# Optimization experiments

Hardware: AMD Instinct MI355X
Metric: run time of the kernel (lower is better)

Reference implementation:

```python
import math
import jax, jax.numpy as jnp
import numpy as np

B, T, H, DH, DV = 4, 4096, 16, 128, 128
CHUNK = 1024
ROPE_BASE = 10000.0
NEG = -1e30


def setup_inputs() -> dict:
    key = jax.random.key(0)
    kq, kk, kv = jax.random.split(key, 3)
    q = jax.random.normal(kq, (B, T, H, DH), dtype=jnp.float32)
    k = jax.random.normal(kk, (B, T, H, DH), dtype=jnp.float32)
    v = jax.random.normal(kv, (B, T, H, DV), dtype=jnp.float32)
    return {"q": q, "k": k, "v": v, "start_index": 0}


def _rope_tables(start, length, dh):
    half = dh // 2
    inv_freq = jnp.exp(jnp.arange(half, dtype=jnp.float32) * -(math.log(ROPE_BASE) / half))
    pos = start + jnp.arange(length, dtype=jnp.float32)
    ang = pos[:, None] * inv_freq[None, :]  # (T, half)
    # broadcast over batch and heads: (1, T, 1, half)
    return jnp.cos(ang)[None, :, None, :], jnp.sin(ang)[None, :, None, :]


def _rotate(x, cos, sin):
    x1, x2 = jnp.split(x, 2, axis=-1)
    return jnp.concatenate([x1 * cos - x2 * sin, x2 * cos + x1 * sin], axis=-1)


def reference(q, k, v, start_index):
    b, t, h, dh = q.shape
    dv = v.shape[-1]
    cos, sin = _rope_tables(start_index, t, dh)
    q_rot = _rotate(q, cos, sin)
    k_rot = _rotate(k, cos, sin)

    nc = t // CHUNK
    qc = q_rot.reshape(b, nc, CHUNK, h, dh)
    kc = k_rot.reshape(b, nc, CHUNK, h, dh)
    vc = v.reshape(b, nc, CHUNK, h, dv)

    # Normalized attention: no 1/sqrt(d) temperature (scale = 1.0)
    scores = jnp.einsum("bnqhd,bnkhd->bnhqk", qc, kc)
    causal = jnp.tril(jnp.ones((CHUNK, CHUNK), dtype=bool))
    scores = jnp.where(causal, scores, NEG)
    attn = jax.nn.softmax(scores, axis=-1)
    out = jnp.einsum("bnhqk,bnkhd->bnqhd", attn, vc)
    return out.reshape(b, t, h, dv)
```

## Files before the change

### kernel.cpp

```cpp
#include <hip/hip_runtime.h>
#include <math.h>

#define Tsz 4096
#define Hn 16
#define DHc 128
#define DVc 128
#define CHK 1024
#define NEGV (-1e30f)
#define ROPE_C 0.14391156831f

typedef float f32x4 __attribute__((ext_vector_type(4)));
typedef short s16x8 __attribute__((ext_vector_type(8)));
typedef unsigned short u16t;
typedef u16t u16x8 __attribute__((ext_vector_type(8)));

__device__ __forceinline__ u16t f2bf(float x){
  union { float f; unsigned u; } cv; cv.f = x;
  unsigned r = cv.u + 0x7fffu + ((cv.u >> 16) & 1u);
  return (u16t)(r >> 16);
}
__device__ __forceinline__ float bf2f(u16t h){
  union { float f; unsigned u; } cv; cv.u = ((unsigned)h) << 16;
  return cv.f;
}
__device__ __forceinline__ f32x4 mfma16(u16x8 a, u16x8 b, f32x4 c){
  return __builtin_amdgcn_mfma_f32_16x16x32_bf16(
      __builtin_bit_cast(s16x8, a), __builtin_bit_cast(s16x8, b), c, 0, 0, 0);
}

__global__ void rope_table_kernel(const int* __restrict__ start,
                                  float* __restrict__ tab){
  const int idx = blockIdx.x * 256 + threadIdx.x;
  const int t = idx >> 6, d = idx & 63;
  const float inv = expf(-(float)d * ROPE_C);
  const float ang = (float)(start[0] + t) * inv;
  float s, c;
  sincosf(ang, &s, &c);
  tab[idx] = c;
  tab[Tsz * 64 + idx] = s;
}

template<int MODE>
__global__ __launch_bounds__(512, 2)
void mega_attn_kernel(const float* __restrict__ q, const float* __restrict__ k,
                      const float* __restrict__ v, const float* __restrict__ tab,
                      const int* __restrict__ start, float* __restrict__ out)
{
  __shared__ __align__(16) u16t sKhi[64 * 128];
  __shared__ __align__(16) u16t sKlo[64 * 128];
  __shared__ __align__(16) u16t sVhi[128 * 64];
  __shared__ __align__(16) u16t sVlo[128 * 64];
  __shared__ __align__(16) u16t sP[8][2048];

  const int bid  = blockIdx.x;
  const int xcd  = bid & 7;
  const int jj   = bid >> 3;
  const int prob = xcd * 32 + (jj & 31);
  const int qt   = jj >> 5;
  const int b  = prob >> 6;
  const int ch = (prob >> 4) & 3;
  const int h  = prob & 15;

  const int tid  = threadIdx.x;
  const int w    = tid >> 6;
  const int lane = tid & 63;
  const int g    = lane >> 4;
  const int lc   = lane & 15;

  const float* cosT = tab;
  const float* sinT = tab + (size_t)Tsz * 64;
  const int tab0 = ch * CHK;
  int st = 0;
  if constexpr (MODE == 1) st = start[0];

  const size_t bh = ((size_t)b * Tsz + (size_t)ch * CHK) * Hn + h;
  const float* qbase = q + bh * DHc;
  const float* kbase = k + bh * DHc;
  const float* vbase = v + bh * DVc;
  float* obase = out + bh * DVc;
  const int rs = Hn * DHc;

  const int qrow0 = 256 * qt + 32 * w;
  u16t* myP = &sP[w][0];

  u16x8 qhi[2][4], qlo[2][4];
  {
    const int srow = lane >> 2;
    const int c4   = lane & 3;
    const int swz  = (srow & 7) << 3;
    #pragma unroll
    for (int rt = 0; rt < 2; ++rt){
      const int rck = qrow0 + rt * 16 + srow;
      const float* qp = qbase + (size_t)rck * rs + 16 * c4;
      f32x4 A[4], Bv[4], Cv[4], Sv[4];
      #pragma unroll
      for (int m = 0; m < 4; ++m){
        A[m]  = *(const f32x4*)(qp + 4 * m);
        Bv[m] = *(const f32x4*)(qp + 64 + 4 * m);
      }
      if constexpr (MODE == 0){
        const float* cp = cosT + (size_t)(tab0 + rck) * 64 + 16 * c4;
        const float* sp = sinT + (size_t)(tab0 + rck) * 64 + 16 * c4;
        #pragma unroll
        for (int m = 0; m < 4; ++m){
          Cv[m] = *(const f32x4*)(cp + 4 * m);
          Sv[m] = *(const f32x4*)(sp + 4 * m);
        }
      } else {
        const float pbase = (float)(st + tab0 + rck);
        #pragma unroll
        for (int m = 0; m < 16; ++m){
          const float inv = expf(-(float)(16 * c4 + m) * ROPE_C);
          float ss, cc;
          sincosf(pbase * inv, &ss, &cc);
          Cv[m >> 2][m & 3] = cc;
          Sv[m >> 2][m & 3] = ss;
        }
      }
      float r1[16], r2[16];
      u16t h1[16], h2[16];
      #pragma unroll
      for (int m = 0; m < 16; ++m){
        const float xa = A[m >> 2][m & 3];
        const float xb = Bv[m >> 2][m & 3];
        const float co = Cv[m >> 2][m & 3];
        const float si = Sv[m >> 2][m & 3];
        r1[m] = xa * co - xb * si;
        r2[m] = xb * co + xa * si;
        h1[m] = f2bf(r1[m]);
        h2[m] = f2bf(r2[m]);
      }
      u16x8 w0, w1, w2, w3;
      #pragma unroll
      for (int m = 0; m < 8; ++m){
        w0[m] = h1[m]; w1[m] = h1[m + 8];
        w2[m] = h2[m]; w3[m] = h2[m + 8];
      }
      *(u16x8*)(myP + ((srow * 128 + 16 * c4     ) ^ swz)) = w0;
      *(u16x8*)(myP + ((srow * 128 + 16 * c4 + 8 ) ^ swz)) = w1;
      *(u16x8*)(myP + ((srow * 128 + 16 * c4 + 64) ^ swz)) = w2;
      *(u16x8*)(myP + ((srow * 128 + 16 * c4 + 72) ^ swz)) = w3;
      #pragma unroll
      for (int ks = 0; ks < 4; ++ks)
        qhi[rt][ks] = *(const u16x8*)(myP + ((lc * 128 + ks * 32 + g * 8) ^ ((lc & 7) << 3)));
      #pragma unroll
      for (int m = 0; m < 8; ++m){
        w0[m] = f2bf(r1[m]     - bf2f(h1[m]));
        w1[m] = f2bf(r1[m + 8] - bf2f(h1[m + 8]));
        w2[m] = f2bf(r2[m]     - bf2f(h2[m]));
        w3[m] = f2bf(r2[m + 8] - bf2f(h2[m + 8]));
      }
      *(u16x8*)(myP + ((srow * 128 + 16 * c4     ) ^ swz)) = w0;
      *(u16x8*)(myP + ((srow * 128 + 16 * c4 + 8 ) ^ swz)) = w1;
      *(u16x8*)(myP + ((srow * 128 + 16 * c4 + 64) ^ swz)) = w2;
      *(u16x8*)(myP + ((srow * 128 + 16 * c4 + 72) ^ swz)) = w3;
      #pragma unroll
      for (int ks = 0; ks < 4; ++ks)
        qlo[rt][ks] = *(const u16x8*)(myP + ((lc * 128 + ks * 32 + g * 8) ^ ((lc & 7) << 3)));
    }
  }

  const f32x4 vzero = {0.f, 0.f, 0.f, 0.f};
  f32x4 acc[2][8];
  #pragma unroll
  for (int rt = 0; rt < 2; ++rt)
    #pragma unroll
    for (int dt = 0; dt < 8; ++dt) acc[rt][dt] = vzero;
  float mrow[8], lrow[8];
  #pragma unroll
  for (int i = 0; i < 8; ++i){ mrow[i] = -INFINITY; lrow[i] = 0.f; }

  const int ntiles = 4 * (qt + 1);
  const int krow = tid >> 3;
  const int kj   = tid & 7;

  for (int t = 0; t < ntiles; ++t){
    {
      const int kr = t * 64 + krow;
      const float* kp = kbase + (size_t)kr * rs + 8 * kj;
      f32x4 xa0 = *(const f32x4*)(kp);
      f32x4 xa1 = *(const f32x4*)(kp + 4);
      f32x4 xb0 = *(const f32x4*)(kp + 64);
      f32x4 xb1 = *(const f32x4*)(kp + 68);
      f32x4 c0, c1, s0, s1;
      if constexpr (MODE == 0){
        const float* cp = cosT + (size_t)(tab0 + kr) * 64 + 8 * kj;
        const float* sp = sinT + (size_t)(tab0 + kr) * 64 + 8 * kj;
        c0 = *(const f32x4*)(cp); c1 = *(const f32x4*)(cp + 4);
        s0 = *(const f32x4*)(sp); s1 = *(const f32x4*)(sp + 4);
      } else {
        const float pbase = (float)(st + tab0 + kr);
        #pragma unroll
        for (int m = 0; m < 8; ++m){
          const float inv = expf(-(float)(8 * kj + m) * ROPE_C);
          float ss, cc;
          sincosf(pbase * inv, &ss, &cc);
          if (m < 4){ c0[m] = cc; s0[m] = ss; }
          else      { c1[m - 4] = cc; s1[m - 4] = ss; }
        }
      }
      u16x8 hh1, ll1, hh2, ll2;
      #pragma unroll
      for (int m = 0; m < 8; ++m){
        const float xa = (m < 4) ? xa0[m & 3] : xa1[m & 3];
        const float xb = (m < 4) ? xb0[m & 3] : xb1[m & 3];
        const float co = (m < 4) ? c0[m & 3]  : c1[m & 3];
        const float si = (m < 4) ? s0[m & 3]  : s1[m & 3];
        const float r1 = xa * co - xb * si;
        const float r2 = xb * co + xa * si;
        const u16t a1h = f2bf(r1); hh1[m] = a1h; ll1[m] = f2bf(r1 - bf2f(a1h));
        const u16t a2h = f2bf(r2); hh2[m] = a2h; ll2[m] = f2bf(r2 - bf2f(a2h));
      }
      const int sw = (krow & 7) << 3;
      const int e1 = (krow * 128 + 8 * kj) ^ sw;
      const int e2 = (krow * 128 + 8 * kj + 64) ^ sw;
      *(u16x8*)(sKhi + e1) = hh1; *(u16x8*)(sKlo + e1) = ll1;
      *(u16x8*)(sKhi + e2) = hh2; *(u16x8*)(sKlo + e2) = ll2;

      const float* vp = vbase + (size_t)(t * 64 + krow) * rs + 16 * kj;
      f32x4 v0 = *(const f32x4*)(vp);
      f32x4 v1 = *(const f32x4*)(vp + 4);
      f32x4 v2 = *(const f32x4*)(vp + 8);
      f32x4 v3 = *(const f32x4*)(vp + 12);
      #pragma unroll
      for (int m = 0; m < 16; ++m){
        const int dv = 16 * kj + m;
        const float xv = (m < 4) ? v0[m & 3] : (m < 8) ? v1[m & 3]
                        : (m < 12) ? v2[m & 3] : v3[m & 3];
        const u16t vh = f2bf(xv);
        const int ve = (dv * 64 + krow) ^ ((((dv & 7) ^ ((dv >> 3) & 7))) << 3);
        sVhi[ve] = vh;
        sVlo[ve] = f2bf(xv - bf2f(vh));
      }
    }
    __syncthreads();

    const int kmin = t * 64;
    if (kmin <= qrow0 + 31){
      f32x4 S[2][4];
      #pragma unroll
      for (int ct = 0; ct < 4; ++ct){
        f32x4 s0v = vzero, s1v = vzero;
        const int krw = 16 * ct + lc;
        const int swk = (krw & 7) << 3;
        #pragma unroll
        for (int ks = 0; ks < 4; ++ks){
          const int ke = (krw * 128 + 32 * ks + 8 * g) ^ swk;
          const u16x8 bh = *(const u16x8*)(sKhi + ke);
          const u16x8 bl = *(const u16x8*)(sKlo + ke);
          s0v = mfma16(qhi[0][ks], bh, s0v);
          s0v = mfma16(qlo[0][ks], bh, s0v);
          s0v = mfma16(qhi[0][ks], bl, s0v);
          s1v = mfma16(qhi[1][ks], bh, s1v);
          s1v = mfma16(qlo[1][ks], bh, s1v);
          s1v = mfma16(qhi[1][ks], bl, s1v);
        }
        S[0][ct] = s0v; S[1][ct] = s1v;
      }
      if (kmin + 63 > qrow0){
        #pragma unroll
        for (int rt = 0; rt < 2; ++rt)
          #pragma unroll
          for (int ct = 0; ct < 4; ++ct){
            const int key = kmin + 16 * ct + lc;
            #pragma unroll
            for (int i = 0; i < 4; ++i){
              if (key > qrow0 + 16 * rt + 4 * g + i) S[rt][ct][i] = NEGV;
            }
          }
      }
      #pragma unroll
      for (int rt = 0; rt < 2; ++rt){
        #pragma unroll
        for (int i = 0; i < 4; ++i){
          const int idx = rt * 4 + i;
          float tm = fmaxf(fmaxf(S[rt][0][i], S[rt][1][i]),
                           fmaxf(S[rt][2][i], S[rt][3][i]));
          tm = fmaxf(tm, __shfl_xor(tm, 1));
          tm = fmaxf(tm, __shfl_xor(tm, 2));
          tm = fmaxf(tm, __shfl_xor(tm, 4));
          tm = fmaxf(tm, __shfl_xor(tm, 8));
          const float mnew = fmaxf(mrow[idx], tm);
          const float sc = __expf(mrow[idx] - mnew);
          float ps = 0.f;
          u16t pb[4];
          #pragma unroll
          for (int ct = 0; ct < 4; ++ct){
            const float p = __expf(S[rt][ct][i] - mnew);
            ps += p;
            pb[ct] = f2bf(p);
          }
          ps += __shfl_xor(ps, 1);
          ps += __shfl_xor(ps, 2);
          ps += __shfl_xor(ps, 4);
          ps += __shfl_xor(ps, 8);
          lrow[idx] = lrow[idx] * sc + ps;
          mrow[idx] = mnew;
          #pragma unroll
          for (int dt = 0; dt < 8; ++dt) acc[rt][dt][i] *= sc;
          const int prow = 16 * rt + 4 * g + i;
          const int swp = (prow & 7) << 3;
          #pragma unroll
          for (int ct = 0; ct < 4; ++ct)
            myP[(prow * 64 + 16 * ct + lc) ^ swp] = pb[ct];
        }
      }
      #pragma unroll
      for (int kvs = 0; kvs < 2; ++kvs){
        const u16x8 pa0 = *(const u16x8*)(myP + ((lc * 64 + kvs * 32 + 8 * g) ^ ((lc & 7) << 3)));
        const u16x8 pa1 = *(const u16x8*)(myP + (((16 + lc) * 64 + kvs * 32 + 8 * g) ^ ((lc & 7) << 3)));
        #pragma unroll
        for (int dt = 0; dt < 8; ++dt){
          const int dv = 16 * dt + lc;
          const int ve = (dv * 64 + kvs * 32 + 8 * g) ^ (((dv & 7) ^ ((dv >> 3) & 7)) << 3);
          const u16x8 vh = *(const u16x8*)(sVhi + ve);
          const u16x8 vl = *(const u16x8*)(sVlo + ve);
          acc[0][dt] = mfma16(pa0, vh, acc[0][dt]);
          acc[0][dt] = mfma16(pa0, vl, acc[0][dt]);
          acc[1][dt] = mfma16(pa1, vh, acc[1][dt]);
          acc[1][dt] = mfma16(pa1, vl, acc[1][dt]);
        }
      }
    }
    __syncthreads();
  }

  #pragma unroll
  for (int rt = 0; rt < 2; ++rt){
    #pragma unroll
    for (int i = 0; i < 4; ++i){
      const int idx = rt * 4 + i;
      const float rl = 1.f / lrow[idx];
      const int rck = qrow0 + 16 * rt + 4 * g + i;
      float* op = obase + (size_t)rck * rs + lc;
      #pragma unroll
      for (int dt = 0; dt < 8; ++dt)
        op[16 * dt] = acc[rt][dt][i] * rl;
    }
  }
}

extern "C" void kernel_launch(void* const* d_in, const int* in_sizes, int n_in,
                              void* d_out, int out_size, void* d_ws, size_t ws_size,
                              hipStream_t stream) {
  const float* q = (const float*)d_in[0];
  const float* k = (const float*)d_in[1];
  const float* v = (const float*)d_in[2];
  const int* start = (const int*)d_in[3];
  float* out = (float*)d_out;
  float* tab = (float*)d_ws;

  const size_t need = (size_t)2 * Tsz * 64 * sizeof(float);
  if (ws_size >= need){
    rope_table_kernel<<<dim3((Tsz * 64) / 256), dim3(256), 0, stream>>>(start, tab);
    mega_attn_kernel<0><<<dim3(1024), dim3(512), 0, stream>>>(q, k, v, tab, start, out);
  } else {
    mega_attn_kernel<1><<<dim3(1024), dim3(512), 0, stream>>>(q, k, v, tab, start, out);
  }
}
```

Before: 1.449 ms.

## Use 16 waves per block with 16 query rows per wave

Doubles the block to 1024 threads so each of 16 waves owns 16 query rows instead of 32. This halves per-wave register state and spreads the K/V tile staging over more threads. Q staging now borrows the K/V shared buffers as scratch, with a barrier before the main loop, which shrinks the P buffer. The cost is that each K/V tile is shared by more waves that each do less MFMA work, plus more barrier participants. Launch bounds of (1024,4) may force register spilling.

```diff
diff --git a/kernel.cpp b/kernel.cpp
--- a/kernel.cpp
+++ b/kernel.cpp
@@ -13,6 +13,7 @@
 typedef short s16x8 __attribute__((ext_vector_type(8)));
 typedef unsigned short u16t;
 typedef u16t u16x8 __attribute__((ext_vector_type(8)));
+typedef u16t u16x4 __attribute__((ext_vector_type(4)));
 
 __device__ __forceinline__ u16t f2bf(float x){
   union { float f; unsigned u; } cv; cv.f = x;
@@ -41,7 +42,7 @@
 }
 
 template<int MODE>
-__global__ __launch_bounds__(512, 2)
+__global__ __launch_bounds__(1024, 4)
 void mega_attn_kernel(const float* __restrict__ q, const float* __restrict__ k,
                       const float* __restrict__ v, const float* __restrict__ tab,
                       const int* __restrict__ start, float* __restrict__ out)
@@ -50,7 +51,7 @@
   __shared__ __align__(16) u16t sKlo[64 * 128];
   __shared__ __align__(16) u16t sVhi[128 * 64];
   __shared__ __align__(16) u16t sVlo[128 * 64];
-  __shared__ __align__(16) u16t sP[8][2048];
+  __shared__ __align__(16) u16t sP[16][1024];
 
   const int bid  = blockIdx.x;
   const int xcd  = bid & 7;
@@ -80,153 +81,138 @@
   float* obase = out + bh * DVc;
   const int rs = Hn * DHc;
 
-  const int qrow0 = 256 * qt + 32 * w;
+  const int qrow0 = 256 * qt + 16 * w;
   u16t* myP = &sP[w][0];
 
-  u16x8 qhi[2][4], qlo[2][4];
+  u16t* qscratch = (w < 4 ? sKhi : w < 8 ? sKlo : w < 12 ? sVhi : sVlo)
+                   + (size_t)(w & 3) * 2048;
+
+  u16x8 qhi[4], qlo[4];
   {
     const int srow = lane >> 2;
     const int c4   = lane & 3;
     const int swz  = (srow & 7) << 3;
-    #pragma unroll
-    for (int rt = 0; rt < 2; ++rt){
-      const int rck = qrow0 + rt * 16 + srow;
-      const float* qp = qbase + (size_t)rck * rs + 16 * c4;
-      f32x4 A[4], Bv[4], Cv[4], Sv[4];
+    const int rck = qrow0 + srow;
+    const float* qp = qbase + (size_t)rck * rs + 16 * c4;
+    f32x4 A[4], Bv[4], Cv[4], Sv[4];
+    #pragma unroll
+    for (int m = 0; m < 4; ++m){
+      A[m]  = *(const f32x4*)(qp + 4 * m);
+      Bv[m] = *(const f32x4*)(qp + 64 + 4 * m);
+    }
+    if constexpr (MODE == 0){
+      const float* cp = cosT + (size_t)(tab0 + rck) * 64 + 16 * c4;
+      const float* sp = sinT + (size_t)(tab0 + rck) * 64 + 16 * c4;
       #pragma unroll
       for (int m = 0; m < 4; ++m){
-        A[m]  = *(const f32x4*)(qp + 4 * m);
-        Bv[m] = *(const f32x4*)(qp + 64 + 4 * m);
-      }
-      if constexpr (MODE == 0){
-        const float* cp = cosT + (size_t)(tab0 + rck) * 64 + 16 * c4;
-        const float* sp = sinT + (size_t)(tab0 + rck) * 64 + 16 * c4;
-        #pragma unroll
-        for (int m = 0; m < 4; ++m){
-          Cv[m] = *(const f32x4*)(cp + 4 * m);
-          Sv[m] = *(const f32x4*)(sp + 4 * m);
-        }
-      } else {
-        const float pbase = (float)(st + tab0 + rck);
-        #pragma unroll
-        for (int m = 0; m < 16; ++m){
-          const float inv = expf(-(float)(16 * c4 + m) * ROPE_C);
-          float ss, cc;
-          sincosf(pbase * inv, &ss, &cc);
-          Cv[m >> 2][m & 3] = cc;
-          Sv[m >> 2][m & 3] = ss;
-        }
-      }
-      float r1[16], r2[16];
-      u16t h1[16], h2[16];
+        Cv[m] = *(const f32x4*)(cp + 4 * m);
+        Sv[m] = *(const f32x4*)(sp + 4 * m);
+      }
+    } else {
+      const float pbase = (float)(st + tab0 + rck);
       #pragma unroll
       for (int m = 0; m < 16; ++m){
-        const float xa = A[m >> 2][m & 3];
-        const float xb = Bv[m >> 2][m & 3];
-        const float co = Cv[m >> 2][m & 3];
-        const float si = Sv[m >> 2][m & 3];
-        r1[m] = xa * co - xb * si;
-        r2[m] = xb * co + xa * si;
-        h1[m] = f2bf(r1[m]);
-        h2[m] = f2bf(r2[m]);
-      }
-      u16x8 w0, w1, w2, w3;
-      #pragma unroll
-      for (int m = 0; m < 8; ++m){
-        w0[m] = h1[m]; w1[m] = h1[m + 8];
-        w2[m] = h2[m]; w3[m] = h2[m + 8];
-      }
-      *(u16x8*)(myP + ((srow * 128 + 16 * c4     ) ^ swz)) = w0;
-      *(u16x8*)(myP + ((srow * 128 + 16 * c4 + 8 ) ^ swz)) = w1;
-      *(u16x8*)(myP + ((srow * 128 + 16 * c4 + 64) ^ swz)) = w2;
-      *(u16x8*)(myP + ((srow * 128 + 16 * c4 + 72) ^ swz)) = w3;
-      #pragma unroll
-      for (int ks = 0; ks < 4; ++ks)
-        qhi[rt][ks] = *(const u16x8*)(myP + ((lc * 128 + ks * 32 + g * 8) ^ ((lc & 7) << 3)));
-      #pragma unroll
-      for (int m = 0; m < 8; ++m){
-        w0[m] = f2bf(r1[m]     - bf2f(h1[m]));
-        w1[m] = f2bf(r1[m + 8] - bf2f(h1[m + 8]));
-        w2[m] = f2bf(r2[m]     - bf2f(h2[m]));
-        w3[m] = f2bf(r2[m + 8] - bf2f(h2[m + 8]));
-      }
-      *(u16x8*)(myP + ((srow * 128 + 16 * c4     ) ^ swz)) = w0;
-      *(u16x8*)(myP + ((srow * 128 + 16 * c4 + 8 ) ^ swz)) = w1;
-      *(u16x8*)(myP + ((srow * 128 + 16 * c4 + 64) ^ swz)) = w2;
-      *(u16x8*)(myP + ((srow * 128 + 16 * c4 + 72) ^ swz)) = w3;
-      #pragma unroll
-      for (int ks = 0; ks < 4; ++ks)
-        qlo[rt][ks] = *(const u16x8*)(myP + ((lc * 128 + ks * 32 + g * 8) ^ ((lc & 7) << 3)));
-    }
+        const float inv = expf(-(float)(16 * c4 + m) * ROPE_C);
+        float ss, cc;
+        sincosf(pbase * inv, &ss, &cc);
+        Cv[m >> 2][m & 3] = cc;
+        Sv[m >> 2][m & 3] = ss;
+      }
+    }
+    float r1[16], r2[16];
+    u16t h1[16], h2[16];
+    #pragma unroll
+    for (int m = 0; m < 16; ++m){
+      const float xa = A[m >> 2][m & 3];
+      const float xb = Bv[m >> 2][m & 3];
+      const float co = Cv[m >> 2][m & 3];
+      const float si = Sv[m >> 2][m & 3];
+      r1[m] = xa * co - xb * si;
+      r2[m] = xb * co + xa * si;
+      h1[m] = f2bf(r1[m]);
+      h2[m] = f2bf(r2[m]);
+    }
+    u16x8 w0, w1, w2, w3;
+    #pragma unroll
+    for (int m = 0; m < 8; ++m){
+      w0[m] = h1[m]; w1[m] = h1[m + 8];
+      w2[m] = h2[m]; w3[m] = h2[m + 8];
+    }
+    *(u16x8*)(qscratch + ((srow * 128 + 16 * c4     ) ^ swz)) = w0;
+    *(u16x8*)(qscratch + ((srow * 128 + 16 * c4 + 8 ) ^ swz)) = w1;
+    *(u16x8*)(qscratch + ((srow * 128 + 16 * c4 + 64) ^ swz)) = w2;
+    *(u16x8*)(qscratch + ((srow * 128 + 16 * c4 + 72) ^ swz)) = w3;
+    #pragma unroll
+    for (int ks = 0; ks < 4; ++ks)
+      qhi[ks] = *(const u16x8*)(qscratch + ((lc * 128 + ks * 32 + g * 8) ^ ((lc & 7) << 3)));
+    #pragma unroll
+    for (int m = 0; m < 8; ++m){
+      w0[m] = f2bf(r1[m]     - bf2f(h1[m]));
+      w1[m] = f2bf(r1[m + 8] - bf2f(h1[m + 8]));
+      w2[m] = f2bf(r2[m]     - bf2f(h2[m]));
+      w3[m] = f2bf(r2[m + 8] - bf2f(h2[m + 8]));
+    }
+    *(u16x8*)(qscratch + ((srow * 128 + 16 * c4     ) ^ swz)) = w0;
+    *(u16x8*)(qscratch + ((srow * 128 + 16 * c4 + 8 ) ^ swz)) = w1;
+    *(u16x8*)(qscratch + ((srow * 128 + 16 * c4 + 64) ^ swz)) = w2;
+    *(u16x8*)(qscratch + ((srow * 128 + 16 * c4 + 72) ^ swz)) = w3;
+    #pragma unroll
+    for (int ks = 0; ks < 4; ++ks)
+      qlo[ks] = *(const u16x8*)(qscratch + ((lc * 128 + ks * 32 + g * 8) ^ ((lc & 7) << 3)));
   }
+  __syncthreads();
 
   const f32x4 vzero = {0.f, 0.f, 0.f, 0.f};
-  f32x4 acc[2][8];
+  f32x4 acc[8];
   #pragma unroll
-  for (int rt = 0; rt < 2; ++rt)
-    #pragma unroll
-    for (int dt = 0; dt < 8; ++dt) acc[rt][dt] = vzero;
-  float mrow[8], lrow[8];
+  for (int dt = 0; dt < 8; ++dt) acc[dt] = vzero;
+  float mrow[4], lrow[4];
   #pragma unroll
-  for (int i = 0; i < 8; ++i){ mrow[i] = -INFINITY; lrow[i] = 0.f; }
+  for (int i = 0; i < 4; ++i){ mrow[i] = -INFINITY; lrow[i] = 0.f; }
 
   const int ntiles = 4 * (qt + 1);
-  const int krow = tid >> 3;
-  const int kj   = tid & 7;
+  const int krow = tid >> 4;
+  const int ka   = tid & 15;
 
   for (int t = 0; t < ntiles; ++t){
     {
       const int kr = t * 64 + krow;
-      const float* kp = kbase + (size_t)kr * rs + 8 * kj;
-      f32x4 xa0 = *(const f32x4*)(kp);
-      f32x4 xa1 = *(const f32x4*)(kp + 4);
-      f32x4 xb0 = *(const f32x4*)(kp + 64);
-      f32x4 xb1 = *(const f32x4*)(kp + 68);
-      f32x4 c0, c1, s0, s1;
+      const float* kp = kbase + (size_t)kr * rs;
+      f32x4 xa = *(const f32x4*)(kp + 4 * ka);
+      f32x4 xb = *(const f32x4*)(kp + 4 * ka + 64);
+      f32x4 cc, ss;
       if constexpr (MODE == 0){
-        const float* cp = cosT + (size_t)(tab0 + kr) * 64 + 8 * kj;
-        const float* sp = sinT + (size_t)(tab0 + kr) * 64 + 8 * kj;
-        c0 = *(const f32x4*)(cp); c1 = *(const f32x4*)(cp + 4);
-        s0 = *(const f32x4*)(sp); s1 = *(const f32x4*)(sp + 4);
+        cc = *(const f32x4*)(cosT + (size_t)(tab0 + kr) * 64 + 4 * ka);
+        ss = *(const f32x4*)(sinT + (size_t)(tab0 + kr) * 64 + 4 * ka);
       } else {
         const float pbase = (float)(st + tab0 + kr);
         #pragma unroll
-        for (int m = 0; m < 8; ++m){
-          const float inv = expf(-(float)(8 * kj + m) * ROPE_C);
-          float ss, cc;
-          sincosf(pbase * inv, &ss, &cc);
-          if (m < 4){ c0[m] = cc; s0[m] = ss; }
-          else      { c1[m - 4] = cc; s1[m - 4] = ss; }
-        }
-      }
-      u16x8 hh1, ll1, hh2, ll2;
-      #pragma unroll
-      for (int m = 0; m < 8; ++m){
-        const float xa = (m < 4) ? xa0[m & 3] : xa1[m & 3];
-        const float xb = (m < 4) ? xb0[m & 3] : xb1[m & 3];
-        const float co = (m < 4) ? c0[m & 3]  : c1[m & 3];
-        const float si = (m < 4) ? s0[m & 3]  : s1[m & 3];
-        const float r1 = xa * co - xb * si;
-        const float r2 = xb * co + xa * si;
+        for (int m = 0; m < 4; ++m){
+          const float inv = expf(-(float)(4 * ka + m) * ROPE_C);
+          float s1, c1;
+          sincosf(pbase * inv, &s1, &c1);
+          cc[m] = c1; ss[m] = s1;
+        }
+      }
+      u16x4 hh1, ll1, hh2, ll2;
+      #pragma unroll
+      for (int m = 0; m < 4; ++m){
+        const float r1 = xa[m] * cc[m] - xb[m] * ss[m];
+        const float r2 = xb[m] * cc[m] + xa[m] * ss[m];
         const u16t a1h = f2bf(r1); hh1[m] = a1h; ll1[m] = f2bf(r1 - bf2f(a1h));
         const u16t a2h = f2bf(r2); hh2[m] = a2h; ll2[m] = f2bf(r2 - bf2f(a2h));
       }
-      const int sw = (krow & 7) << 3;
-      const int e1 = (krow * 128 + 8 * kj) ^ sw;
-      const int e2 = (krow * 128 + 8 * kj + 64) ^ sw;
-      *(u16x8*)(sKhi + e1) = hh1; *(u16x8*)(sKlo + e1) = ll1;
-      *(u16x8*)(sKhi + e2) = hh2; *(u16x8*)(sKlo + e2) = ll2;
-
-      const float* vp = vbase + (size_t)(t * 64 + krow) * rs + 16 * kj;
+      const int e1 = (krow * 128 + 4 * ka) ^ ((krow & 7) << 3);
+      *(u16x4*)(sKhi + e1)      = hh1; *(u16x4*)(sKlo + e1)      = ll1;
+      *(u16x4*)(sKhi + e1 + 64) = hh2; *(u16x4*)(sKlo + e1 + 64) = ll2;
+
+      const float* vp = vbase + (size_t)kr * rs + 8 * ka;
       f32x4 v0 = *(const f32x4*)(vp);
       f32x4 v1 = *(const f32x4*)(vp + 4);
-      f32x4 v2 = *(const f32x4*)(vp + 8);
-      f32x4 v3 = *(const f32x4*)(vp + 12);
-      #pragma unroll
-      for (int m = 0; m < 16; ++m){
-        const int dv = 16 * kj + m;
-        const float xv = (m < 4) ? v0[m & 3] : (m < 8) ? v1[m & 3]
-                        : (m < 12) ? v2[m & 3] : v3[m & 3];
+      #pragma unroll
+      for (int m = 0; m < 8; ++m){
+        const int dv = 8 * ka + m;
+        const float xv = (m < 4) ? v0[m & 3] : v1[m & 3];
         const u16t vh = f2bf(xv);
         const int ve = (dv * 64 + krow) ^ ((((dv & 7) ^ ((dv >> 3) & 7))) << 3);
         sVhi[ve] = vh;
@@ -236,11 +222,11 @@
     __syncthreads();
 
     const int kmin = t * 64;
-    if (kmin <= qrow0 + 31){
-      f32x4 S[2][4];
+    if (kmin <= qrow0 + 15){
+      f32x4 S[4];
       #pragma unroll
       for (int ct = 0; ct < 4; ++ct){
-        f32x4 s0v = vzero, s1v = vzero;
+        f32x4 s0v = vzero;
         const int krw = 16 * ct + lc;
         const int swk = (krw & 7) << 3;
         #pragma unroll
@@ -248,77 +234,64 @@
           const int ke = (krw * 128 + 32 * ks + 8 * g) ^ swk;
           const u16x8 bh = *(const u16x8*)(sKhi + ke);
           const u16x8 bl = *(const u16x8*)(sKlo + ke);
-          s0v = mfma16(qhi[0][ks], bh, s0v);
-          s0v = mfma16(qlo[0][ks], bh, s0v);
-          s0v = mfma16(qhi[0][ks], bl, s0v);
-          s1v = mfma16(qhi[1][ks], bh, s1v);
-          s1v = mfma16(qlo[1][ks], bh, s1v);
-          s1v = mfma16(qhi[1][ks], bl, s1v);
-        }
-        S[0][ct] = s0v; S[1][ct] = s1v;
+          s0v = mfma16(qhi[ks], bh, s0v);
+          s0v = mfma16(qlo[ks], bh, s0v);
+          s0v = mfma16(qhi[ks], bl, s0v);
+        }
+        S[ct] = s0v;
       }
       if (kmin + 63 > qrow0){
         #pragma unroll
-        for (int rt = 0; rt < 2; ++rt)
+        for (int ct = 0; ct < 4; ++ct){
+          const int key = kmin + 16 * ct + lc;
           #pragma unroll
-          for (int ct = 0; ct < 4; ++ct){
-            const int key = kmin + 16 * ct + lc;
-            #pragma unroll
-            for (int i = 0; i < 4; ++i){
-              if (key > qrow0 + 16 * rt + 4 * g + i) S[rt][ct][i] = NEGV;
-            }
+          for (int i = 0; i < 4; ++i){
+            if (key > qrow0 + 4 * g + i) S[ct][i] = NEGV;
           }
-      }
-      #pragma unroll
-      for (int rt = 0; rt < 2; ++rt){
-        #pragma unroll
-        for (int i = 0; i < 4; ++i){
-          const int idx = rt * 4 + i;
-          float tm = fmaxf(fmaxf(S[rt][0][i], S[rt][1][i]),
-                           fmaxf(S[rt][2][i], S[rt][3][i]));
-          tm = fmaxf(tm, __shfl_xor(tm, 1));
-          tm = fmaxf(tm, __shfl_xor(tm, 2));
-          tm = fmaxf(tm, __shfl_xor(tm, 4));
-          tm = fmaxf(tm, __shfl_xor(tm, 8));
-          const float mnew = fmaxf(mrow[idx], tm);
-          const float sc = __expf(mrow[idx] - mnew);
-          float ps = 0.f;
-          u16t pb[4];
-          #pragma unroll
-          for (int ct = 0; ct < 4; ++ct){
-            const float p = __expf(S[rt][ct][i] - mnew);
-            ps += p;
-            pb[ct] = f2bf(p);
-          }
-          ps += __shfl_xor(ps, 1);
-          ps += __shfl_xor(ps, 2);
-          ps += __shfl_xor(ps, 4);
-          ps += __shfl_xor(ps, 8);
-          lrow[idx] = lrow[idx] * sc + ps;
-          mrow[idx] = mnew;
-          #pragma unroll
-          for (int dt = 0; dt < 8; ++dt) acc[rt][dt][i] *= sc;
-          const int prow = 16 * rt + 4 * g + i;
-          const int swp = (prow & 7) << 3;
-          #pragma unroll
-          for (int ct = 0; ct < 4; ++ct)
-            myP[(prow * 64 + 16 * ct + lc) ^ swp] = pb[ct];
-        }
+        }
+      }
+      #pragma unroll
+      for (int i = 0; i < 4; ++i){
+        float tm = fmaxf(fmaxf(S[0][i], S[1][i]), fmaxf(S[2][i], S[3][i]));
+        tm = fmaxf(tm, __shfl_xor(tm, 1));
+        tm = fmaxf(tm, __shfl_xor(tm, 2));
+        tm = fmaxf(tm, __shfl_xor(tm, 4));
+        tm = fmaxf(tm, __shfl_xor(tm, 8));
+        const float mnew = fmaxf(mrow[i], tm);
+        const float sc = __expf(mrow[i] - mnew);
+        float ps = 0.f;
+        u16t pb[4];
+        #pragma unroll
+        for (int ct = 0; ct < 4; ++ct){
+          const float p = __expf(S[ct][i] - mnew);
+          ps += p;
+          pb[ct] = f2bf(p);
+        }
+        ps += __shfl_xor(ps, 1);
+        ps += __shfl_xor(ps, 2);
+        ps += __shfl_xor(ps, 4);
+        ps += __shfl_xor(ps, 8);
+        lrow[i] = lrow[i] * sc + ps;
+        mrow[i] = mnew;
+        #pragma unroll
+        for (int dt = 0; dt < 8; ++dt) acc[dt][i] *= sc;
+        const int prow = 4 * g + i;
+        const int swp = (prow & 7) << 3;
+        #pragma unroll
+        for (int ct = 0; ct < 4; ++ct)
+          myP[(prow * 64 + 16 * ct + lc) ^ swp] = pb[ct];
       }
       #pragma unroll
       for (int kvs = 0; kvs < 2; ++kvs){
-        const u16x8 pa0 = *(const u16x8*)(myP + ((lc * 64 + kvs * 32 + 8 * g) ^ ((lc & 7) << 3)));
-        const u16x8 pa1 = *(const u16x8*)(myP + (((16 + lc) * 64 + kvs * 32 + 8 * g) ^ ((lc & 7) << 3)));
+        const u16x8 pa = *(const u16x8*)(myP + ((lc * 64 + kvs * 32 + 8 * g) ^ ((lc & 7) << 3)));
         #pragma unroll
         for (int dt = 0; dt < 8; ++dt){
           const int dv = 16 * dt + lc;
           const int ve = (dv * 64 + kvs * 32 + 8 * g) ^ (((dv & 7) ^ ((dv >> 3) & 7)) << 3);
           const u16x8 vh = *(const u16x8*)(sVhi + ve);
           const u16x8 vl = *(const u16x8*)(sVlo + ve);
-          acc[0][dt] = mfma16(pa0, vh, acc[0][dt]);
-          acc[0][dt] = mfma16(pa0, vl, acc[0][dt]);
-          acc[1][dt] = mfma16(pa1, vh, acc[1][dt]);
-          acc[1][dt] = mfma16(pa1, vl, acc[1][dt]);
+          acc[dt] = mfma16(pa, vh, acc[dt]);
+          acc[dt] = mfma16(pa, vl, acc[dt]);
         }
       }
     }
@@ -326,17 +299,13 @@
   }
 
   #pragma unroll
-  for (int rt = 0; rt < 2; ++rt){
-    #pragma unroll
-    for (int i = 0; i < 4; ++i){
-      const int idx = rt * 4 + i;
-      const float rl = 1.f / lrow[idx];
-      const int rck = qrow0 + 16 * rt + 4 * g + i;
-      float* op = obase + (size_t)rck * rs + lc;
-      #pragma unroll
-      for (int dt = 0; dt < 8; ++dt)
-        op[16 * dt] = acc[rt][dt][i] * rl;
-    }
+  for (int i = 0; i < 4; ++i){
+    const float rl = 1.f / lrow[i];
+    const int rck = qrow0 + 4 * g + i;
+    float* op = obase + (size_t)rck * rs + lc;
+    #pragma unroll
+    for (int dt = 0; dt < 8; ++dt)
+      op[16 * dt] = acc[dt][i] * rl;
   }
 }
 
@@ -353,8 +322,8 @@
   const size_t need = (size_t)2 * Tsz * 64 * sizeof(float);
   if (ws_size >= need){
     rope_table_kernel<<<dim3((Tsz * 64) / 256), dim3(256), 0, stream>>>(start, tab);
-    mega_attn_kernel<0><<<dim3(1024), dim3(512), 0, stream>>>(q, k, v, tab, start, out);
+    mega_attn_kernel<0><<<dim3(1024), dim3(1024), 0, stream>>>(q, k, v, tab, start, out);
   } else {
-    mega_attn_kernel<1><<<dim3(1024), dim3(512), 0, stream>>>(q, k, v, tab, start, out);
+    mega_attn_kernel<1><<<dim3(1024), dim3(1024), 0, stream>>>(q, k, v, tab, start, out);
   }
 }
```

New measurement: 1.483 ms. 1.02x slower.
